# Kernel tuning notes

Hardware: AMD Instinct MI355X
Metric: run time of the kernel (lower is better)

The kernel has to match this reference:

```python
import jax, jax.numpy as jnp
import numpy as np

N = 8192
K = 30


def setup_inputs() -> dict:
    key = jax.random.key(0)
    k1, k2, k3 = jax.random.split(key, 3)
    estimate = jax.random.normal(k1, (N, K), dtype=jnp.float32)
    event_time = jax.random.uniform(k2, (N,), dtype=jnp.float32) * 30.0
    event = (jax.random.uniform(k3, (N,)) < 0.7).astype(jnp.float32)
    target = jnp.stack([event_time, event], axis=1)  # [N, 2]
    intervals = (jnp.arange(K, dtype=jnp.float32) + 0.5)  # midpoints per init_kwargs
    return {"estimate": estimate, "target": target, "intervals": intervals}


def reference(estimate, target, intervals):
    event_time = target[:, 0]
    event = target[:, 1] != 0
    # hazard -> survival via exclusive cumprod (pad with 1 at the front)
    hazard = jax.nn.sigmoid(estimate)                       # [N, K]
    surv = jnp.cumprod(1.0 - hazard, axis=-1)               # inclusive cumprod
    surv_prev = jnp.concatenate(
        [jnp.ones_like(surv[..., :1]), surv[..., :-1]], axis=-1
    )                                                       # S(t_{k-1}), exclusive
    pdf = hazard * surv_prev                                # [N, K]
    mrl = jnp.sum(intervals * pdf, axis=-1)                 # [N]
    # comparable pairs: i has an event and t_i < t_j
    comparable = (event_time[:, None] < event_time[None, :]) & event[:, None]
    diff = mrl[:, None] - mrl[None, :]                      # [N, N]
    cnt = jnp.sum(comparable).astype(diff.dtype)
    return jnp.sum(jnp.where(comparable, diff, 0.0)) / cnt
```

## Files before the change

kernel.cpp:

```cpp
#include <hip/hip_runtime.h>
#include <math.h>

constexpr int N = 8192;
constexpr int K = 30;
constexpr int TPB = 256;
constexpr int NI_BLOCKS = N / TPB;
constexpr int NJ_SLICES = 32;
constexpr int JSPAN = N / NJ_SLICES;
constexpr int NBLOCKS2 = NI_BLOCKS * NJ_SLICES;


__global__ void mrl_kernel(const float* __restrict__ est,
                           const float* __restrict__ intervals,
                           float* __restrict__ mrl) {
    int i = blockIdx.x * blockDim.x + threadIdx.x;
    if (i >= N) return;
    const float* e = est + i * K;
    double sp = 1.0;
    double m  = 0.0;
#pragma unroll
    for (int k = 0; k < K; ++k) {
        float hf = 1.0f / (1.0f + __expf(-e[k]));
        double h = (double)hf;
        m += (double)intervals[k] * h * sp;
        sp *= (1.0 - h);
    }
    mrl[i] = (float)m;
}

__global__ void pair_kernel(const float* __restrict__ target,
                            const float* __restrict__ mrl,
                            double* __restrict__ pnum,
                            int* __restrict__ pcnt) {
    __shared__ float  s_t[JSPAN];
    __shared__ float  s_m[JSPAN];
    __shared__ double r_num[TPB];
    __shared__ int    r_cnt[TPB];

    const int tid = threadIdx.x;
    const int ib  = blockIdx.x / NJ_SLICES;
    const int js  = blockIdx.x % NJ_SLICES;
    const int i   = ib * TPB + tid;
    const int j   = js * JSPAN + tid;

    const float2 tgt = ((const float2*)target)[i];
    const float  ti  = tgt.x;
    const bool   ei  = (tgt.y != 0.0f);
    const float  mi  = mrl[i];

    const float2 tj = ((const float2*)target)[j];
    s_t[tid] = tj.x;
    s_m[tid] = mrl[j];
    __syncthreads();

    const float4* s_t4 = (const float4*)s_t;
    const float4* s_m4 = (const float4*)s_m;

    double smj = 0.0;
    int c0 = 0, c1 = 0, c2 = 0, c3 = 0;

#pragma unroll
    for (int ch = 0; ch < JSPAN / 64; ++ch) {
        float a0 = 0.f, a1 = 0.f, a2 = 0.f, a3 = 0.f;
#pragma unroll
        for (int q = 0; q < 16; ++q) {
            const int jj4 = ch * 16 + q;
            float4 tv = s_t4[jj4];
            float4 mv = s_m4[jj4];
            bool b0 = ti < tv.x, b1 = ti < tv.y, b2 = ti < tv.z, b3 = ti < tv.w;
            c0 += b0; a0 += b0 ? mv.x : 0.0f;
            c1 += b1; a1 += b1 ? mv.y : 0.0f;
            c2 += b2; a2 += b2 ? mv.z : 0.0f;
            c3 += b3; a3 += b3 ? mv.w : 0.0f;
        }
        smj += (double)((a0 + a1) + (a2 + a3));
    }

    const int cnt = (c0 + c1) + (c2 + c3);
    r_num[tid] = ei ? ((double)cnt * (double)mi - smj) : 0.0;
    r_cnt[tid] = ei ? cnt : 0;
    __syncthreads();
    for (int s = TPB / 2; s > 0; s >>= 1) {
        if (tid < s) {
            r_num[tid] += r_num[tid + s];
            r_cnt[tid] += r_cnt[tid + s];
        }
        __syncthreads();
    }
    if (tid == 0) {
        pnum[blockIdx.x] = r_num[0];
        pcnt[blockIdx.x] = r_cnt[0];
    }
}

__global__ void final_kernel(const double* __restrict__ pnum,
                             const int* __restrict__ pcnt,
                             float* __restrict__ out) {
    __shared__ double r_num[TPB];
    __shared__ int    r_cnt[TPB];
    const int tid = threadIdx.x;
    double n = 0.0;
    int    c = 0;
#pragma unroll
    for (int p = 0; p < NBLOCKS2 / TPB; ++p) {
        const int idx = p * TPB + tid;
        n += pnum[idx];
        c += pcnt[idx];
    }
    r_num[tid] = n;
    r_cnt[tid] = c;
    __syncthreads();
    for (int s = TPB / 2; s > 0; s >>= 1) {
        if (tid < s) {
            r_num[tid] += r_num[tid + s];
            r_cnt[tid] += r_cnt[tid + s];
        }
        __syncthreads();
    }
    if (tid == 0) out[0] = (float)(r_num[0] / (double)r_cnt[0]);
}

extern "C" void kernel_launch(void* const* d_in, const int* in_sizes, int n_in,
                              void* d_out, int out_size, void* d_ws, size_t ws_size,
                              hipStream_t stream) {
    const float* est       = (const float*)d_in[0];
    const float* target    = (const float*)d_in[1];
    const float* intervals = (const float*)d_in[2];
    float* out = (float*)d_out;

    float*  mrl  = (float*)d_ws;
    double* pnum = (double*)((char*)d_ws + 32768);
    int*    pcnt = (int*)((char*)d_ws + 40960);

    mrl_kernel<<<64, 128, 0, stream>>>(est, intervals, mrl);
    pair_kernel<<<NBLOCKS2, TPB, 0, stream>>>(target, mrl, pnum, pcnt);
    final_kernel<<<1, TPB, 0, stream>>>(pnum, pcnt, out);
}
```

Measured before the change: 20.25 us.

## Fuse MRL, pair and final reduction into one kernel with ticket-based last-block reduce

Merges the three kernels into a single launch. Each block recomputes the MRL values for its own i and j rows instead of reading them from a precomputed buffer, and the last block to finish, found through an atomic ticket, performs the final reduction. This removes two kernel launches and the global round-trip for MRL. In exchange the MRL work is done about 64 times over, each row recomputed by 32 blocks on both the i and j sides, and a memset plus a threadfence and atomic are added.

```diff
diff --git a/kernel.cpp b/kernel.cpp
--- a/kernel.cpp
+++ b/kernel.cpp
@@ -1,56 +1,68 @@
 #include <hip/hip_runtime.h>
 #include <math.h>
 
-constexpr int N = 8192;
-constexpr int K = 30;
+constexpr int N   = 8192;
+constexpr int K   = 30;
 constexpr int TPB = 256;
-constexpr int NI_BLOCKS = N / TPB;
-constexpr int NJ_SLICES = 32;
-constexpr int JSPAN = N / NJ_SLICES;
-constexpr int NBLOCKS2 = NI_BLOCKS * NJ_SLICES;
+constexpr int NI  = 32;
+constexpr int NJ  = 32;
+constexpr int NBLK = NI * NJ;
 
 
-__global__ void mrl_kernel(const float* __restrict__ est,
-                           const float* __restrict__ intervals,
-                           float* __restrict__ mrl) {
-    int i = blockIdx.x * blockDim.x + threadIdx.x;
-    if (i >= N) return;
-    const float* e = est + i * K;
-    double sp = 1.0;
-    double m  = 0.0;
+__device__ __forceinline__ double mrl_row(const float* __restrict__ est,
+                                          const float* __restrict__ intervals,
+                                          int row) {
+    const float2* e2 = (const float2*)(est + row * K);
+    double sp = 1.0, m = 0.0;
 #pragma unroll
-    for (int k = 0; k < K; ++k) {
-        float hf = 1.0f / (1.0f + __expf(-e[k]));
-        double h = (double)hf;
-        m += (double)intervals[k] * h * sp;
-        sp *= (1.0 - h);
+    for (int k2 = 0; k2 < K / 2; ++k2) {
+        float2 ev = e2[k2];
+        float h0f = 1.0f / (1.0f + __expf(-ev.x));
+        float h1f = 1.0f / (1.0f + __expf(-ev.y));
+        double h0 = (double)h0f, h1 = (double)h1f;
+        m += (double)intervals[2 * k2] * h0 * sp;
+        sp *= (1.0 - h0);
+        m += (double)intervals[2 * k2 + 1] * h1 * sp;
+        sp *= (1.0 - h1);
     }
-    mrl[i] = (float)m;
+    return m;
 }
 
-__global__ void pair_kernel(const float* __restrict__ target,
-                            const float* __restrict__ mrl,
-                            double* __restrict__ pnum,
-                            int* __restrict__ pcnt) {
-    __shared__ float  s_t[JSPAN];
-    __shared__ float  s_m[JSPAN];
+__global__ void fused_kernel(const float* __restrict__ est,
+                             const float* __restrict__ target,
+                             const float* __restrict__ intervals,
+                             int* __restrict__ ticket,
+                             double* __restrict__ pnum,
+                             int* __restrict__ pcnt,
+                             float* __restrict__ out) {
+    __shared__ float  s_t[TPB];
+    __shared__ float  s_m[TPB];
     __shared__ double r_num[TPB];
     __shared__ int    r_cnt[TPB];
+    __shared__ int    s_flag;
 
     const int tid = threadIdx.x;
-    const int ib  = blockIdx.x / NJ_SLICES;
-    const int js  = blockIdx.x % NJ_SLICES;
+    const int bid = blockIdx.x;
+    const int ib  = bid >> 5;
+    const int js  = bid & 31;
     const int i   = ib * TPB + tid;
-    const int j   = js * JSPAN + tid;
+    const int j   = js * TPB + tid;
 
-    const float2 tgt = ((const float2*)target)[i];
-    const float  ti  = tgt.x;
-    const bool   ei  = (tgt.y != 0.0f);
-    const float  mi  = mrl[i];
+    const float2 ti2 = ((const float2*)target)[i];
+    const float  ti  = ti2.x;
+    const bool   ei  = (ti2.y != 0.0f);
 
-    const float2 tj = ((const float2*)target)[j];
-    s_t[tid] = tj.x;
-    s_m[tid] = mrl[j];
+    const double mi_d = mrl_row(est, intervals, i);
+    float mj;
+    if (ib == js) {
+        mj = (float)mi_d;
+    } else {
+        mj = (float)mrl_row(est, intervals, j);
+    }
+    const float mi = (float)mi_d;
+
+    s_t[tid] = ((const float2*)target)[j].x;
+    s_m[tid] = mj;
     __syncthreads();
 
     const float4* s_t4 = (const float4*)s_t;
@@ -60,7 +72,7 @@
     int c0 = 0, c1 = 0, c2 = 0, c3 = 0;
 
 #pragma unroll
-    for (int ch = 0; ch < JSPAN / 64; ++ch) {
+    for (int ch = 0; ch < TPB / 64; ++ch) {
         float a0 = 0.f, a1 = 0.f, a2 = 0.f, a3 = 0.f;
 #pragma unroll
         for (int q = 0; q < 16; ++q) {
@@ -87,37 +99,37 @@
         }
         __syncthreads();
     }
+
     if (tid == 0) {
-        pnum[blockIdx.x] = r_num[0];
-        pcnt[blockIdx.x] = r_cnt[0];
+        pnum[bid] = r_num[0];
+        pcnt[bid] = r_cnt[0];
+        __threadfence();
+        int old = atomicAdd(ticket, 1);
+        s_flag = (old == NBLK - 1);
     }
-}
+    __syncthreads();
 
-__global__ void final_kernel(const double* __restrict__ pnum,
-                             const int* __restrict__ pcnt,
-                             float* __restrict__ out) {
-    __shared__ double r_num[TPB];
-    __shared__ int    r_cnt[TPB];
-    const int tid = threadIdx.x;
-    double n = 0.0;
-    int    c = 0;
+    if (s_flag) {
+        __threadfence();
+        double n = 0.0;
+        int    c = 0;
 #pragma unroll
-    for (int p = 0; p < NBLOCKS2 / TPB; ++p) {
-        const int idx = p * TPB + tid;
-        n += pnum[idx];
-        c += pcnt[idx];
+        for (int p = 0; p < NBLK / TPB; ++p) {
+            n += pnum[p * TPB + tid];
+            c += pcnt[p * TPB + tid];
+        }
+        r_num[tid] = n;
+        r_cnt[tid] = c;
+        __syncthreads();
+        for (int s = TPB / 2; s > 0; s >>= 1) {
+            if (tid < s) {
+                r_num[tid] += r_num[tid + s];
+                r_cnt[tid] += r_cnt[tid + s];
+            }
+            __syncthreads();
+        }
+        if (tid == 0) out[0] = (float)(r_num[0] / (double)r_cnt[0]);
     }
-    r_num[tid] = n;
-    r_cnt[tid] = c;
-    __syncthreads();
-    for (int s = TPB / 2; s > 0; s >>= 1) {
-        if (tid < s) {
-            r_num[tid] += r_num[tid + s];
-            r_cnt[tid] += r_cnt[tid + s];
-        }
-        __syncthreads();
-    }
-    if (tid == 0) out[0] = (float)(r_num[0] / (double)r_cnt[0]);
 }
 
 extern "C" void kernel_launch(void* const* d_in, const int* in_sizes, int n_in,
@@ -128,11 +140,11 @@
     const float* intervals = (const float*)d_in[2];
     float* out = (float*)d_out;
 
-    float*  mrl  = (float*)d_ws;
-    double* pnum = (double*)((char*)d_ws + 32768);
-    int*    pcnt = (int*)((char*)d_ws + 40960);
+    int*    ticket = (int*)d_ws;
+    double* pnum   = (double*)((char*)d_ws + 16);
+    int*    pcnt   = (int*)((char*)d_ws + 16 + 8192);
 
-    mrl_kernel<<<64, 128, 0, stream>>>(est, intervals, mrl);
-    pair_kernel<<<NBLOCKS2, TPB, 0, stream>>>(target, mrl, pnum, pcnt);
-    final_kernel<<<1, TPB, 0, stream>>>(pnum, pcnt, out);
+    (void)hipMemsetAsync(d_ws, 0, 4, stream);
+    fused_kernel<<<NBLK, TPB, 0, stream>>>(est, target, intervals,
+                                           ticket, pnum, pcnt, out);
 }
```

After: 46.29 us. 129% more time.

## Process two i rows per thread in pair kernel and stage mrl inputs in LDS

Applied to the files above, without the earlier changes.

The pair kernel now has each thread handle two i elements against a 128-wide j slice. Each shared-memory load of t and m then feeds twice the compare/accumulate work, and the grid stays at 1024 blocks. The mrl kernel now stages each block's estimate rows into LDS with coalesced float2 loads instead of strided per-thread row reads, and launches 32 blocks of 256 threads. The costs are more registers per thread and only half the threads filling the shared j tile.

```diff
diff --git a/kernel.cpp b/kernel.cpp
--- a/kernel.cpp
+++ b/kernel.cpp
@@ -1,23 +1,34 @@
 #include <hip/hip_runtime.h>
 #include <math.h>
 
-constexpr int N = 8192;
-constexpr int K = 30;
-constexpr int TPB = 256;
-constexpr int NI_BLOCKS = N / TPB;
-constexpr int NJ_SLICES = 32;
-constexpr int JSPAN = N / NJ_SLICES;
-constexpr int NBLOCKS2 = NI_BLOCKS * NJ_SLICES;
+constexpr int N    = 8192;
+constexpr int K    = 30;
+constexpr int TPB  = 256;
+constexpr int IPT  = 2;
+constexpr int ISPAN = TPB * IPT;
+constexpr int NI   = N / ISPAN;
+constexpr int NJ   = 64;
+constexpr int JSPAN = N / NJ;
+constexpr int NBLK = NI * NJ;
 
 
 __global__ void mrl_kernel(const float* __restrict__ est,
                            const float* __restrict__ intervals,
                            float* __restrict__ mrl) {
-    int i = blockIdx.x * blockDim.x + threadIdx.x;
-    if (i >= N) return;
-    const float* e = est + i * K;
-    double sp = 1.0;
-    double m  = 0.0;
+    __shared__ float s_est[TPB * K];
+
+    const int tid  = threadIdx.x;
+    const int row0 = blockIdx.x * TPB;
+
+    const float2* src = (const float2*)(est + (size_t)row0 * K);
+    float2* dst = (float2*)s_est;
+#pragma unroll
+    for (int t = 0; t < (TPB * K) / (2 * TPB); ++t)
+        dst[t * TPB + tid] = src[t * TPB + tid];
+    __syncthreads();
+
+    const float* e = s_est + tid * K;
+    double sp = 1.0, m = 0.0;
 #pragma unroll
     for (int k = 0; k < K; ++k) {
         float hf = 1.0f / (1.0f + __expf(-e[k]));
@@ -25,7 +36,7 @@
         m += (double)intervals[k] * h * sp;
         sp *= (1.0 - h);
     }
-    mrl[i] = (float)m;
+    mrl[row0 + tid] = (float)m;
 }
 
 __global__ void pair_kernel(const float* __restrict__ target,
@@ -38,47 +49,72 @@
     __shared__ int    r_cnt[TPB];
 
     const int tid = threadIdx.x;
-    const int ib  = blockIdx.x / NJ_SLICES;
-    const int js  = blockIdx.x % NJ_SLICES;
-    const int i   = ib * TPB + tid;
-    const int j   = js * JSPAN + tid;
+    const int bid = blockIdx.x;
+    const int ib  = bid >> 6;
+    const int js  = bid & (NJ - 1);
 
-    const float2 tgt = ((const float2*)target)[i];
-    const float  ti  = tgt.x;
-    const bool   ei  = (tgt.y != 0.0f);
-    const float  mi  = mrl[i];
+    const int i0 = ib * ISPAN + tid;
+    const int i1 = i0 + TPB;
 
-    const float2 tj = ((const float2*)target)[j];
-    s_t[tid] = tj.x;
-    s_m[tid] = mrl[j];
+    const float2 t0v = ((const float2*)target)[i0];
+    const float2 t1v = ((const float2*)target)[i1];
+    const float ti0 = t0v.x;  const bool e0 = (t0v.y != 0.0f);
+    const float ti1 = t1v.x;  const bool e1 = (t1v.y != 0.0f);
+    const float mi0 = mrl[i0];
+    const float mi1 = mrl[i1];
+
+    if (tid < JSPAN) {
+        const int j = js * JSPAN + tid;
+        s_t[tid] = ((const float2*)target)[j].x;
+        s_m[tid] = mrl[j];
+    }
     __syncthreads();
 
     const float4* s_t4 = (const float4*)s_t;
     const float4* s_m4 = (const float4*)s_m;
 
-    double smj = 0.0;
-    int c0 = 0, c1 = 0, c2 = 0, c3 = 0;
+    double smj0 = 0.0, smj1 = 0.0;
+    int c00 = 0, c01 = 0, c02 = 0, c03 = 0;
+    int c10 = 0, c11 = 0, c12 = 0, c13 = 0;
 
 #pragma unroll
     for (int ch = 0; ch < JSPAN / 64; ++ch) {
-        float a0 = 0.f, a1 = 0.f, a2 = 0.f, a3 = 0.f;
+        float a00 = 0.f, a01 = 0.f, a02 = 0.f, a03 = 0.f;
+        float a10 = 0.f, a11 = 0.f, a12 = 0.f, a13 = 0.f;
 #pragma unroll
         for (int q = 0; q < 16; ++q) {
             const int jj4 = ch * 16 + q;
             float4 tv = s_t4[jj4];
             float4 mv = s_m4[jj4];
-            bool b0 = ti < tv.x, b1 = ti < tv.y, b2 = ti < tv.z, b3 = ti < tv.w;
-            c0 += b0; a0 += b0 ? mv.x : 0.0f;
-            c1 += b1; a1 += b1 ? mv.y : 0.0f;
-            c2 += b2; a2 += b2 ? mv.z : 0.0f;
-            c3 += b3; a3 += b3 ? mv.w : 0.0f;
+            {
+                bool b0 = ti0 < tv.x, b1 = ti0 < tv.y, b2 = ti0 < tv.z, b3 = ti0 < tv.w;
+                c00 += b0; a00 += b0 ? mv.x : 0.0f;
+                c01 += b1; a01 += b1 ? mv.y : 0.0f;
+                c02 += b2; a02 += b2 ? mv.z : 0.0f;
+                c03 += b3; a03 += b3 ? mv.w : 0.0f;
+            }
+            {
+                bool b0 = ti1 < tv.x, b1 = ti1 < tv.y, b2 = ti1 < tv.z, b3 = ti1 < tv.w;
+                c10 += b0; a10 += b0 ? mv.x : 0.0f;
+                c11 += b1; a11 += b1 ? mv.y : 0.0f;
+                c12 += b2; a12 += b2 ? mv.z : 0.0f;
+                c13 += b3; a13 += b3 ? mv.w : 0.0f;
+            }
         }
-        smj += (double)((a0 + a1) + (a2 + a3));
+        smj0 += (double)((a00 + a01) + (a02 + a03));
+        smj1 += (double)((a10 + a11) + (a12 + a13));
     }
 
-    const int cnt = (c0 + c1) + (c2 + c3);
-    r_num[tid] = ei ? ((double)cnt * (double)mi - smj) : 0.0;
-    r_cnt[tid] = ei ? cnt : 0;
+    const int cnt0 = (c00 + c01) + (c02 + c03);
+    const int cnt1 = (c10 + c11) + (c12 + c13);
+
+    double num = 0.0;
+    int    cnt = 0;
+    if (e0) { num += (double)cnt0 * (double)mi0 - smj0; cnt += cnt0; }
+    if (e1) { num += (double)cnt1 * (double)mi1 - smj1; cnt += cnt1; }
+
+    r_num[tid] = num;
+    r_cnt[tid] = cnt;
     __syncthreads();
     for (int s = TPB / 2; s > 0; s >>= 1) {
         if (tid < s) {
@@ -88,8 +124,8 @@
         __syncthreads();
     }
     if (tid == 0) {
-        pnum[blockIdx.x] = r_num[0];
-        pcnt[blockIdx.x] = r_cnt[0];
+        pnum[bid] = r_num[0];
+        pcnt[bid] = r_cnt[0];
     }
 }
 
@@ -102,7 +138,7 @@
     double n = 0.0;
     int    c = 0;
 #pragma unroll
-    for (int p = 0; p < NBLOCKS2 / TPB; ++p) {
+    for (int p = 0; p < NBLK / TPB; ++p) {
         const int idx = p * TPB + tid;
         n += pnum[idx];
         c += pcnt[idx];
@@ -132,7 +168,7 @@
     double* pnum = (double*)((char*)d_ws + 32768);
     int*    pcnt = (int*)((char*)d_ws + 40960);
 
-    mrl_kernel<<<64, 128, 0, stream>>>(est, intervals, mrl);
-    pair_kernel<<<NBLOCKS2, TPB, 0, stream>>>(target, mrl, pnum, pcnt);
+    mrl_kernel<<<N / TPB, TPB, 0, stream>>>(est, intervals, mrl);
+    pair_kernel<<<NBLK, TPB, 0, stream>>>(target, mrl, pnum, pcnt);
     final_kernel<<<1, TPB, 0, stream>>>(pnum, pcnt, out);
 }
```

Result: no change. 20.42 us (+0.8%).
